# Kernel tuning notes

Hardware: AMD Instinct MI355X
Metric: run time of the kernel (lower is better)

Reference implementation:

```python
import jax, jax.numpy as jnp
import numpy as np
from jax import lax

POOL = 2048      # pool_size
HARD = 128       # hard_slices
EXTRA = 64       # random_extra
T_MIN, T_MAX, T_STEPS = -5.0, 5.0, 17
EPS = 1e-12


def _t_phi():
    t = jnp.linspace(T_MIN, T_MAX, T_STEPS)
    return t, jnp.exp(-0.5 * t * t)


def _slice_losses(z, A, t, phi):
    # z: [B, D], A: [D, M] -> per-slice ECF matching loss [M]
    zc = z - z.mean(axis=0, keepdims=True)
    u = zc @ A                              # [B, M]
    ut = u[:, :, None] * t                  # [B, M, T]
    ecf_re = jnp.cos(ut).mean(axis=0)       # [M, T] (= Re E[exp(i u t)])
    ecf_im = jnp.sin(ut).mean(axis=0)       # [M, T]
    integrand = ((ecf_re - phi) ** 2 + ecf_im ** 2) * phi
    dt = t[1:] - t[:-1]
    # trapezoid rule along t
    return (0.5 * (integrand[..., 1:] + integrand[..., :-1]) * dt).sum(axis=-1)


def _gram_schmidt(H):
    # Sequential Gram-Schmidt over columns of H: [D, m]. Mirrors
    # _gs_select_from_ranked in the generic case (unit random directions
    # never degenerate, so the top-m ranked columns are all kept).
    def body(j, Q):
        v = H[:, j]
        v = v - Q @ (Q.T @ v)   # unfilled cols of Q are zero -> no-op
        n = jnp.linalg.norm(v)
        return Q.at[:, j].set(v / jnp.maximum(n, EPS))
    return lax.fori_loop(0, H.shape[1], body, jnp.zeros_like(H))


def setup_inputs() -> dict:
    key = jax.random.key(0)
    z = jax.random.normal(key, (2048, 1024), dtype=jnp.float32)
    return {"z": z, "seed": 0}


def reference(z, seed):
    B, D = z.shape
    t, phi = _t_phi()

    # random unit-norm direction pool (seeded)
    A_pool = jax.random.normal(jax.random.key(seed), (D, POOL), dtype=z.dtype)
    A_pool = A_pool / (jnp.linalg.norm(A_pool, axis=0, keepdims=True) + EPS)

    # rank slices by ECF loss, take hardest, orthonormalize (hardmaxqr)
    losses = _slice_losses(z, A_pool, t, phi)
    ranked = jnp.argsort(-losses)
    hard_raw = A_pool[:, ranked[:HARD]]     # [D, HARD]
    hard = _gram_schmidt(hard_raw)

    # random extra directions, orthogonalized against hard
    R = jax.random.normal(jax.random.key(seed + 9991), (D, EXTRA), dtype=z.dtype)
    R = R / (jnp.linalg.norm(R, axis=0, keepdims=True) + EPS)
    R = R - hard @ (hard.T @ R)
    R = R / (jnp.linalg.norm(R, axis=0, keepdims=True) + EPS)

    A_final = jnp.concatenate([hard, R], axis=1)   # [D, HARD+EXTRA]
    final_losses = _slice_losses(z, A_final, t, phi)
    return final_losses.mean() * B
```

## Files before the change

kernel.cpp:

```cpp
#include <hip/hip_runtime.h>
#include <cstdint>
#include <cstddef>


#define THREEFRY_PARTITIONABLE 1

static constexpr int B_ = 2048;
static constexpr int D_ = 1024;
static constexpr int P_ = 2048;
static constexpr int HARD_ = 128;
static constexpr int EXTRA_ = 64;
static constexpr int NF_ = 192;
static constexpr int TS_ = 17;

typedef short short8v __attribute__((ext_vector_type(8)));
typedef float f32x4v __attribute__((ext_vector_type(4)));


__device__ __forceinline__ void threefry2x32(uint32_t k0, uint32_t k1,
                                             uint32_t c0, uint32_t c1,
                                             uint32_t& o0, uint32_t& o1) {
  uint32_t ks0 = k0, ks1 = k1, ks2 = 0x1BD11BDAu ^ k0 ^ k1;
  uint32_t x0 = c0 + ks0;
  uint32_t x1 = c1 + ks1;
#define TF_ROT(r) { x0 += x1; x1 = (x1 << (r)) | (x1 >> (32 - (r))); x1 ^= x0; }
  TF_ROT(13) TF_ROT(15) TF_ROT(26) TF_ROT(6)
  x0 += ks1; x1 += ks2 + 1u;
  TF_ROT(17) TF_ROT(29) TF_ROT(16) TF_ROT(24)
  x0 += ks2; x1 += ks0 + 2u;
  TF_ROT(13) TF_ROT(15) TF_ROT(26) TF_ROT(6)
  x0 += ks0; x1 += ks1 + 3u;
  TF_ROT(17) TF_ROT(29) TF_ROT(16) TF_ROT(24)
  x0 += ks1; x1 += ks2 + 4u;
  TF_ROT(13) TF_ROT(15) TF_ROT(26) TF_ROT(6)
  x0 += ks2; x1 += ks0 + 5u;
#undef TF_ROT
  o0 = x0; o1 = x1;
}

__device__ __forceinline__ float bits_to_normal(uint32_t bits) {
  uint32_t fb = (bits >> 9) | 0x3f800000u;
  float f = __uint_as_float(fb) - 1.0f;
  const float lo = -0.99999994f;
  float u = f * 2.0f + lo;
  u = fmaxf(lo, u);
  float w = -log1pf(-u * u);
  float p;
  if (w < 5.0f) {
    w = w - 2.5f;
    p = 2.81022636e-08f;
    p = fmaf(p, w, 3.43273939e-07f);
    p = fmaf(p, w, -3.5233877e-06f);
    p = fmaf(p, w, -4.39150654e-06f);
    p = fmaf(p, w, 0.00021858087f);
    p = fmaf(p, w, -0.00125372503f);
    p = fmaf(p, w, -0.00417768164f);
    p = fmaf(p, w, 0.246640727f);
    p = fmaf(p, w, 1.50140941f);
  } else {
    w = sqrtf(w) - 3.0f;
    p = -0.000200214257f;
    p = fmaf(p, w, 0.000100950558f);
    p = fmaf(p, w, 0.00134934322f);
    p = fmaf(p, w, -0.00367342844f);
    p = fmaf(p, w, 0.00573950773f);
    p = fmaf(p, w, -0.0076224613f);
    p = fmaf(p, w, 0.00943887047f);
    p = fmaf(p, w, 1.00167406f);
    p = fmaf(p, w, 2.83297682f);
  }
  return ((float)1.4142135623730951) * (p * u);
}

__device__ __forceinline__ float tf_normal(uint32_t k0, uint32_t k1,
                                           uint32_t idx) {
#if THREEFRY_PARTITIONABLE
  uint32_t a, b;
  threefry2x32(k0, k1, 0u, idx, a, b);
  return bits_to_normal(a ^ b);
#endif
}


__global__ __launch_bounds__(256) void colsum_part_kernel(const float* __restrict__ Z,
                                                          float* __restrict__ part) {
  int col = blockIdx.x * 256 + threadIdx.x;
  int r0 = blockIdx.y * 64;
  float s = 0.f;
  for (int r = r0; r < r0 + 64; ++r) s += Z[(size_t)r * D_ + col];
  part[blockIdx.y * D_ + col] = s;
}

__global__ __launch_bounds__(256) void colmean_fin_kernel(const float* __restrict__ part,
                                                          float* __restrict__ mean) {
  int col = blockIdx.x * 256 + threadIdx.x;
  float s = 0.f;
  for (int rb = 0; rb < 32; ++rb) s += part[rb * D_ + col];
  mean[col] = s * (1.0f / (float)B_);
}

__global__ __launch_bounds__(256) void gen_pool_norm_kernel(float* __restrict__ AT,
                                                            const int* __restrict__ seedp) {
  const int p = blockIdx.x;
  const int tid = threadIdx.x;
  uint64_t s = (uint64_t)(int64_t)seedp[0];
  uint32_t k0 = (uint32_t)(s >> 32), k1 = (uint32_t)s;
  float v[4]; float ss = 0.f;
#pragma unroll
  for (int q = 0; q < 4; ++q) {
    int d = tid + 256 * q;
    uint32_t i = (uint32_t)((d << 11) + p);
    v[q] = tf_normal(k0, k1, i);
    ss = fmaf(v[q], v[q], ss);
  }
  __shared__ float red[256];
  red[tid] = ss;
  __syncthreads();
  for (int st = 128; st > 0; st >>= 1) { if (tid < st) red[tid] += red[tid + st]; __syncthreads(); }
  float denom = sqrtf(red[0]) + 1e-12f;
#pragma unroll
  for (int q = 0; q < 4; ++q) {
    int d = tid + 256 * q;
    AT[(size_t)p * D_ + d] = v[q] / denom;
  }
}

__global__ __launch_bounds__(256) void gen_R_norm_kernel(float* __restrict__ DIRS,
                                                         const int* __restrict__ seedp) {
  const int j = blockIdx.x;
  const int tid = threadIdx.x;
  uint64_t s = (uint64_t)((int64_t)seedp[0] + 9991);
  uint32_t k0 = (uint32_t)(s >> 32), k1 = (uint32_t)s;
  float v[4]; float ss = 0.f;
#pragma unroll
  for (int q = 0; q < 4; ++q) {
    int d = tid + 256 * q;
    uint32_t i = (uint32_t)((d << 6) + j);
    v[q] = tf_normal(k0, k1, i);
    ss = fmaf(v[q], v[q], ss);
  }
  __shared__ float red[256];
  red[tid] = ss;
  __syncthreads();
  for (int st = 128; st > 0; st >>= 1) { if (tid < st) red[tid] += red[tid + st]; __syncthreads(); }
  float denom = sqrtf(red[0]) + 1e-12f;
#pragma unroll
  for (int q = 0; q < 4; ++q) {
    int d = tid + 256 * q;
    DIRS[(size_t)(HARD_ + j) * D_ + d] = v[q] / denom;
  }
}

__global__ __launch_bounds__(256) void rownorm_kernel(float* __restrict__ Arows, int ncols) {
  float* r = Arows + (size_t)blockIdx.x * ncols;
  int tid = threadIdx.x;
  float ss = 0.f;
  for (int d = tid; d < ncols; d += 256) { float v = r[d]; ss = fmaf(v, v, ss); }
  __shared__ float red[256];
  red[tid] = ss;
  __syncthreads();
  for (int s = 128; s > 0; s >>= 1) { if (tid < s) red[tid] += red[tid + s]; __syncthreads(); }
  float denom = sqrtf(red[0]) + 1e-12f;
  for (int d = tid; d < ncols; d += 256) r[d] = r[d] / denom;
}

__device__ __forceinline__ uint32_t f2bf_rne(float x) {
  uint32_t u = __float_as_uint(x);
  return (u + 0x7fffu + ((u >> 16) & 1u)) >> 16;
}

__global__ __launch_bounds__(512) void gemm_mfma_kernel(const float* __restrict__ A,
                                                        const float* __restrict__ Z,
                                                        const float* __restrict__ meanp,
                                                        float* __restrict__ C) {
  constexpr int BK = 32;
  __shared__ ushort Ah[128][40], Al[128][40], Bh[128][40], Bl[128][40];
  const int tid = threadIdx.x;
  const int lane = tid & 63;
  const int w = tid >> 6;
  const int wr = w >> 2;
  const int wc = w & 3;
  const int m0 = blockIdx.y * 128;
  const int n0 = blockIdx.x * 128;

  f32x4v acc[4][2];
#pragma unroll
  for (int mi = 0; mi < 4; ++mi)
#pragma unroll
    for (int ni = 0; ni < 2; ++ni) acc[mi][ni] = (f32x4v){0.f, 0.f, 0.f, 0.f};

  float4 ra[2], rb[2];
  auto ld = [&](int s) {
    const int k0 = s * BK;
#pragma unroll
    for (int q = 0; q < 2; ++q) {
      int f4 = tid + q * 512;
      int r = f4 >> 3;
      int kq = (f4 & 7) * 4;
      ra[q] = *(const float4*)(A + (size_t)(m0 + r) * D_ + k0 + kq);
      float4 z = *(const float4*)(Z + (size_t)(n0 + r) * D_ + k0 + kq);
      float4 mu = *(const float4*)(meanp + k0 + kq);
      rb[q] = make_float4(z.x - mu.x, z.y - mu.y, z.z - mu.z, z.w - mu.w);
    }
  };
  auto st = [&]() {
#pragma unroll
    for (int q = 0; q < 2; ++q) {
      int f4 = tid + q * 512;
      int r = f4 >> 3;
      int kq = (f4 & 7) * 4;
      float av[4] = {ra[q].x, ra[q].y, ra[q].z, ra[q].w};
      float bv[4] = {rb[q].x, rb[q].y, rb[q].z, rb[q].w};
      ushort ah[4], al[4], bh[4], bl[4];
#pragma unroll
      for (int c = 0; c < 4; ++c) {
        uint32_t h = f2bf_rne(av[c]);
        ah[c] = (ushort)h;
        al[c] = (ushort)f2bf_rne(av[c] - __uint_as_float(h << 16));
        uint32_t g = f2bf_rne(bv[c]);
        bh[c] = (ushort)g;
        bl[c] = (ushort)f2bf_rne(bv[c] - __uint_as_float(g << 16));
      }
      *(ushort4*)&Ah[r][kq] = make_ushort4(ah[0], ah[1], ah[2], ah[3]);
      *(ushort4*)&Al[r][kq] = make_ushort4(al[0], al[1], al[2], al[3]);
      *(ushort4*)&Bh[r][kq] = make_ushort4(bh[0], bh[1], bh[2], bh[3]);
      *(ushort4*)&Bl[r][kq] = make_ushort4(bl[0], bl[1], bl[2], bl[3]);
    }
  };
  auto compute = [&]() {
    const int rl = lane & 15;
    const int koff = (lane >> 4) * 8;
    short8v a_h[4], a_l[4], b_h[2], b_l[2];
#pragma unroll
    for (int mi = 0; mi < 4; ++mi) {
      int arow = wr * 64 + mi * 16 + rl;
      a_h[mi] = *(const short8v*)&Ah[arow][koff];
      a_l[mi] = *(const short8v*)&Al[arow][koff];
    }
#pragma unroll
    for (int ni = 0; ni < 2; ++ni) {
      int brow = wc * 32 + ni * 16 + rl;
      b_h[ni] = *(const short8v*)&Bh[brow][koff];
      b_l[ni] = *(const short8v*)&Bl[brow][koff];
    }
#pragma unroll
    for (int mi = 0; mi < 4; ++mi)
#pragma unroll
      for (int ni = 0; ni < 2; ++ni) {
        acc[mi][ni] = __builtin_amdgcn_mfma_f32_16x16x32_bf16(a_h[mi], b_h[ni], acc[mi][ni], 0, 0, 0);
        acc[mi][ni] = __builtin_amdgcn_mfma_f32_16x16x32_bf16(a_h[mi], b_l[ni], acc[mi][ni], 0, 0, 0);
        acc[mi][ni] = __builtin_amdgcn_mfma_f32_16x16x32_bf16(a_l[mi], b_h[ni], acc[mi][ni], 0, 0, 0);
      }
  };

  const int nst = D_ / BK;
  ld(0);
  for (int s = 0; s < nst; ++s) {
    if (s) __syncthreads();
    st();
    __syncthreads();
    if (s + 1 < nst) ld(s + 1);
    compute();
  }

  const int rl = lane & 15;
  const int rq = (lane >> 4) * 4;
#pragma unroll
  for (int mi = 0; mi < 4; ++mi)
#pragma unroll
    for (int ni = 0; ni < 2; ++ni) {
      int col = n0 + wc * 32 + ni * 16 + rl;
#pragma unroll
      for (int r = 0; r < 4; ++r) {
        int row = m0 + wr * 64 + mi * 16 + rq + r;
        C[(size_t)row * B_ + col] = acc[mi][ni][r];
      }
    }
}

template <int BM, int BN, int BK, int TM, int TN, int NT, bool CENTER_B>
__global__ __launch_bounds__(NT) void gemm_nt_kernel(const float* __restrict__ A,
                                                     const float* __restrict__ Bm,
                                                     const float* __restrict__ meanp,
                                                     float* __restrict__ C,
                                                     int M, int N, int K,
                                                     int lda, int ldb, int ldc) {
  static_assert(TN == 4 || TN == 8, "");
  static_assert((BM * BK) % (4 * NT) == 0, "");
  __shared__ float As[2][BK][BM + 4];
  __shared__ float Bs[2][BK][BN + 4];
  const int tid = threadIdx.x;
  constexpr int TX = BN / TN;
  constexpr int TY = NT / TX;
  static_assert(TY * TM == BM, "");
  const int tx = tid % TX;
  const int ty = tid / TX;
  const int m0 = blockIdx.y * BM;
  const int n0 = blockIdx.x * BN;
  constexpr int NF4 = (BM * BK) / (4 * NT);
  constexpr int F4R = BK / 4;

  float acc[TM][TN];
#pragma unroll
  for (int i = 0; i < TM; ++i)
#pragma unroll
    for (int j = 0; j < TN; ++j) acc[i][j] = 0.f;

  float4 ra[NF4], rb[NF4];

  auto ldnext = [&](int k0) {
#pragma unroll
    for (int q = 0; q < NF4; ++q) {
      int idx = tid + q * NT;
      int r = idx / F4R;
      int kk = (idx % F4R) * 4;
      ra[q] = *(const float4*)(A + (size_t)(m0 + r) * lda + k0 + kk);
      float4 b = *(const float4*)(Bm + (size_t)(n0 + r) * ldb + k0 + kk);
      if constexpr (CENTER_B) {
        float4 mu = *(const float4*)(meanp + k0 + kk);
        b = make_float4(b.x - mu.x, b.y - mu.y, b.z - mu.z, b.w - mu.w);
      }
      rb[q] = b;
    }
  };
  auto stnext = [&](int buf) {
#pragma unroll
    for (int q = 0; q < NF4; ++q) {
      int idx = tid + q * NT;
      int r = idx / F4R;
      int kk = (idx % F4R) * 4;
      As[buf][kk + 0][r] = ra[q].x; As[buf][kk + 1][r] = ra[q].y;
      As[buf][kk + 2][r] = ra[q].z; As[buf][kk + 3][r] = ra[q].w;
      Bs[buf][kk + 0][r] = rb[q].x; Bs[buf][kk + 1][r] = rb[q].y;
      Bs[buf][kk + 2][r] = rb[q].z; Bs[buf][kk + 3][r] = rb[q].w;
    }
  };
  auto compute = [&](int buf) {
#pragma unroll
    for (int kk = 0; kk < BK; ++kk) {
      float a[TM], b[TN];
#pragma unroll
      for (int q = 0; q < TM / 4; ++q) {
        float4 v = *(const float4*)&As[buf][kk][ty * TM + q * 4];
        a[q * 4 + 0] = v.x; a[q * 4 + 1] = v.y; a[q * 4 + 2] = v.z; a[q * 4 + 3] = v.w;
      }
      {
        float4 v = *(const float4*)&Bs[buf][kk][tx * 4];
        b[0] = v.x; b[1] = v.y; b[2] = v.z; b[3] = v.w;
      }
      if constexpr (TN == 8) {
        float4 v = *(const float4*)&Bs[buf][kk][BN / 2 + tx * 4];
        b[4] = v.x; b[5] = v.y; b[6] = v.z; b[7] = v.w;
      }
#pragma unroll
      for (int i = 0; i < TM; ++i)
#pragma unroll
        for (int j = 0; j < TN; ++j) acc[i][j] = fmaf(a[i], b[j], acc[i][j]);
    }
  };

  ldnext(0);
  stnext(0);
  __syncthreads();
  const int nst = K / BK;
  for (int s = 0; s < nst; ++s) {
    const int cur = s & 1;
    if (s + 1 < nst) ldnext((s + 1) * BK);
    compute(cur);
    if (s + 1 < nst) stnext(cur ^ 1);
    __syncthreads();
  }

#pragma unroll
  for (int i = 0; i < TM; ++i) {
    const int gm = m0 + ty * TM + i;
    float4 c0 = make_float4(acc[i][0], acc[i][1], acc[i][2], acc[i][3]);
    *(float4*)(C + (size_t)gm * ldc + n0 + tx * 4) = c0;
    if constexpr (TN == 8) {
      float4 c1 = make_float4(acc[i][4], acc[i][5], acc[i][6], acc[i][7]);
      *(float4*)(C + (size_t)gm * ldc + n0 + BN / 2 + tx * 4) = c1;
    }
  }
}

__global__ __launch_bounds__(256) void gram_kernel(const float* __restrict__ A,
                                                   const float* __restrict__ Bm,
                                                   float* __restrict__ C,
                                                   int K, int ldc) {
  __shared__ float As[32][136];
  __shared__ float BsT[128][36];
  const int tid = threadIdx.x;
  const int i0 = blockIdx.y * 32;
  const int j0 = blockIdx.x * 32;
  const int i = tid >> 3;
  const int jl = (tid & 7) * 4;

  float s[4][4];
#pragma unroll
  for (int m = 0; m < 4; ++m)
#pragma unroll
    for (int c = 0; c < 4; ++c) s[m][c] = 0.f;

  for (int kc = 0; kc < K; kc += 128) {
#pragma unroll
    for (int q = 0; q < 4; ++q) {
      int f4 = tid + 256 * q;
      int r = f4 >> 5;
      int kq = (f4 & 31) * 4;
      float4 va = *(const float4*)(A + (size_t)(i0 + r) * K + kc + kq);
      *(float4*)&As[r][kq] = va;
      float4 vb = *(const float4*)(Bm + (size_t)(j0 + r) * K + kc + kq);
      BsT[kq + 0][r] = vb.x; BsT[kq + 1][r] = vb.y;
      BsT[kq + 2][r] = vb.z; BsT[kq + 3][r] = vb.w;
    }
    __syncthreads();
    for (int k4 = 0; k4 < 128; k4 += 4) {
#pragma unroll
      for (int c = 0; c < 4; ++c) {
        int k = k4 + c;
        float a = As[i][k];
        float4 b = *(const float4*)&BsT[k][jl];
        s[0][c] = fmaf(a, b.x, s[0][c]);
        s[1][c] = fmaf(a, b.y, s[1][c]);
        s[2][c] = fmaf(a, b.z, s[2][c]);
        s[3][c] = fmaf(a, b.w, s[3][c]);
      }
    }
    __syncthreads();
  }
#pragma unroll
  for (int m = 0; m < 4; ++m)
    C[(size_t)(i0 + i) * ldc + j0 + jl + m] = (s[m][0] + s[m][1]) + (s[m][2] + s[m][3]);
}

__global__ __launch_bounds__(256) void ecf_loss_kernel(const float* __restrict__ U,
                                                       float* __restrict__ out_loss) {
  const float* u = U + (size_t)blockIdx.x * B_;
  const int tid = threadIdx.x;
  float sc[TS_], ss[TS_];
#pragma unroll
  for (int k = 0; k < TS_; ++k) { sc[k] = 0.f; ss[k] = 0.f; }

  for (int b = tid; b < B_; b += 256) {
    float x = u[b];
#pragma unroll
    for (int k = 0; k < TS_; ++k) {
      const double tk = -5.0 + 0.625 * (double)k;
      const float trev = (float)(tk * 0.15915494309189535);
      float r = x * trev;
      sc[k] += __builtin_amdgcn_cosf(r);
      ss[k] += __builtin_amdgcn_sinf(r);
    }
  }
#pragma unroll
  for (int k = 0; k < TS_; ++k) {
#pragma unroll
    for (int off = 32; off > 0; off >>= 1) {
      sc[k] += __shfl_down(sc[k], off, 64);
      ss[k] += __shfl_down(ss[k], off, 64);
    }
  }
  __shared__ float rsc[4][TS_], rss[4][TS_];
  int wid = tid >> 6, lane = tid & 63;
  if (lane == 0) {
#pragma unroll
    for (int k = 0; k < TS_; ++k) { rsc[wid][k] = sc[k]; rss[wid][k] = ss[k]; }
  }
  __syncthreads();
  if (tid == 0) {
    float loss = 0.f, prevI = 0.f;
#pragma unroll
    for (int k = 0; k < TS_; ++k) {
      float tk = -5.0f + 0.625f * (float)k;
      float phik = expf(-0.5f * tk * tk);
      float S = (rsc[0][k] + rsc[1][k]) + (rsc[2][k] + rsc[3][k]);
      float T = (rss[0][k] + rss[1][k]) + (rss[2][k] + rss[3][k]);
      float re = S * (1.0f / (float)B_) - phik;
      float im = T * (1.0f / (float)B_);
      float I = (re * re + im * im) * phik;
      if (k > 0) loss += 0.5f * (I + prevI) * 0.625f;
      prevI = I;
    }
    out_loss[blockIdx.x] = loss;
  }
}

__global__ __launch_bounds__(1024) void sort_kernel(const float* __restrict__ loss,
                                                    int* __restrict__ ranked) {
  __shared__ float ls[P_];
  __shared__ int li[P_];
  int tid = threadIdx.x;
  for (int i = tid; i < P_; i += 1024) { ls[i] = loss[i]; li[i] = i; }
  __syncthreads();
  for (int k = 2; k <= P_; k <<= 1) {
    for (int j = k >> 1; j > 0; j >>= 1) {
      for (int i = tid; i < P_; i += 1024) {
        int ixj = i ^ j;
        if (ixj > i) {
          bool up = ((i & k) == 0);
          float la = ls[i], lb = ls[ixj];
          int ia = li[i], ib = li[ixj];
          bool a_after_b = (la < lb) || (la == lb && ia > ib);
          bool sw = up ? a_after_b : (!a_after_b && !(la == lb && ia == ib));
          if (sw) { ls[i] = lb; ls[ixj] = la; li[i] = ib; li[ixj] = ia; }
        }
      }
      __syncthreads();
    }
  }
  for (int i = tid; i < P_; i += 1024) ranked[i] = li[i];
}

__global__ __launch_bounds__(256) void gather_ht_kernel(const float* __restrict__ AT,
                                                        const int* __restrict__ ranked,
                                                        float* __restrict__ HT) {
  int j = blockIdx.x;
  int src = ranked[j];
  for (int d = threadIdx.x; d < D_; d += 256)
    HT[(size_t)j * D_ + d] = AT[(size_t)src * D_ + d];
}

__global__ __launch_bounds__(512) void chol_inv_kernel(const float* __restrict__ G,
                                                       float* __restrict__ W) {
  __shared__ float g[HARD_][HARD_ + 1];
  __shared__ float w[HARD_][HARD_ + 1];
  __shared__ float m[16][16 * 7 + 4];
  __shared__ float rinv[HARD_];
  const int tid = threadIdx.x;

  for (int idx = tid; idx < HARD_ * HARD_; idx += 512)
    g[idx >> 7][idx & 127] = G[idx];
  for (int idx = tid; idx < HARD_ * (HARD_ + 1); idx += 512)
    (&w[0][0])[idx] = 0.f;
  __syncthreads();

  const int bcol = tid & 127;
  const int aoff = tid >> 7;
  for (int K = 0; K < 8; ++K) {
    const int b = K << 4;
    const int c0 = b + 16;
    const int nc = HARD_ - c0;

    if (tid < 16) {
      const int j = tid;
      float c[16];
#pragma unroll
      for (int k = 0; k < 16; ++k) c[k] = g[b + k][b + j];
#pragma unroll
      for (int i = 0; i < 16; ++i) {
        float rii = sqrtf(__shfl(c[i], i, 16));
        float rinvi = 1.0f / rii;
        float rij = c[i] * rinvi;
        if (j > i) c[i] = rij;
        if (j == i) c[i] = rii;
#pragma unroll
        for (int a = i + 1; a < 16; ++a) {
          float ria = __shfl(c[i], a, 16);
          if (j >= a) c[a] = fmaf(-ria, rij, c[a]);
        }
      }
#pragma unroll
      for (int k = 0; k < 16; ++k) if (k <= j) g[b + k][b + j] = c[k];
      rinv[b + j] = 1.0f / c[j];
    }
    __syncthreads();

    if (nc > 0) {
      if (tid < nc) {
        const int j = c0 + tid;
        float x[16];
#pragma unroll
        for (int i = 0; i < 16; ++i) {
          float acc = g[b + i][j];
#pragma unroll
          for (int m2 = 0; m2 < i; ++m2)
            acc = fmaf(-g[b + m2][b + i], x[m2], acc);
          x[i] = acc * rinv[b + i];
        }
#pragma unroll
        for (int i = 0; i < 16; ++i) g[b + i][j] = x[i];
      }
      __syncthreads();

      if (bcol >= c0) {
        float rkb[16];
#pragma unroll
        for (int k = 0; k < 16; ++k) rkb[k] = g[b + k][bcol];
        for (int a = c0 + aoff; a <= bcol; a += 4) {
          float acc = g[a][bcol];
#pragma unroll
          for (int k = 0; k < 16; ++k)
            acc = fmaf(-g[b + k][a], rkb[k], acc);
          g[a][bcol] = acc;
        }
      }
    }
    __syncthreads();
  }

  if (tid < HARD_) {
    const int blk = tid >> 4, j = tid & 15, b = blk << 4;
    const float myrinv = rinv[b + j];
    float wcol[16];
#pragma unroll
    for (int i = 15; i >= 0; --i) {
      float s = 0.f;
#pragma unroll
      for (int k = 15; k > i; --k) s = fmaf(g[b + i][b + k], wcol[k], s);
      float v = -rinv[b + i] * s;
      wcol[i] = (i < j) ? v : ((i == j) ? myrinv : 0.f);
    }
#pragma unroll
    for (int k = 0; k < 16; ++k) w[b + k][b + j] = wcol[k];
  }
  __syncthreads();

  for (int I = 6; I >= 0; --I) {
    const int b = I << 4;
    const int c0 = b + 16;
    const int nc = HARD_ - c0;
    const int nel = 16 * nc;
    for (int e = tid; e < nel; e += 512) {
      int r = e / nc, c = e - r * nc;
      float acc = 0.f;
      for (int k = c0; k < HARD_; ++k)
        acc = fmaf(g[b + r][k], w[k][c0 + c], acc);
      m[r][c] = acc;
    }
    __syncthreads();
    for (int e = tid; e < nel; e += 512) {
      int r = e / nc, c = e - r * nc;
      float acc = 0.f;
#pragma unroll
      for (int rp = 0; rp < 16; ++rp)
        acc = fmaf(w[b + r][b + rp], m[rp][c], acc);
      w[b + r][c0 + c] = -acc;
    }
    __syncthreads();
  }

  for (int idx = tid; idx < HARD_ * HARD_; idx += 512)
    W[idx] = w[idx >> 7][idx & 127];
}

__global__ __launch_bounds__(128) void apply_winv_kernel(const float* __restrict__ HT,
                                                         const float* __restrict__ W,
                                                         float* __restrict__ DIRS) {
  int j = blockIdx.y;
  int d = blockIdx.x * 128 + threadIdx.x;
  __shared__ float wc[HARD_];
  for (int i = threadIdx.x; i <= j; i += 128) wc[i] = W[i * HARD_ + j];
  __syncthreads();
  float acc = 0.f;
  for (int i = 0; i <= j; ++i) acc = fmaf(wc[i], HT[(size_t)i * D_ + d], acc);
  DIRS[(size_t)j * D_ + d] = acc;
}

__global__ __launch_bounds__(128) void proj_update_kernel(float* __restrict__ DIRS,
                                                          const float* __restrict__ C) {
  int j = blockIdx.y;
  int d = blockIdx.x * 128 + threadIdx.x;
  __shared__ float cc[HARD_];
  cc[threadIdx.x] = C[threadIdx.x * EXTRA_ + j];
  if (threadIdx.x + 128 < HARD_) cc[threadIdx.x + 128] = C[(threadIdx.x + 128) * EXTRA_ + j];
  __syncthreads();
  float acc = DIRS[(size_t)(HARD_ + j) * D_ + d];
  for (int i = 0; i < HARD_; ++i) acc = fmaf(-cc[i], DIRS[(size_t)i * D_ + d], acc);
  DIRS[(size_t)(HARD_ + j) * D_ + d] = acc;
}

__global__ __launch_bounds__(256) void finalize_kernel(const float* __restrict__ FL,
                                                       float* __restrict__ out) {
  __shared__ float red[256];
  int tid = threadIdx.x;
  red[tid] = (tid < NF_) ? FL[tid] : 0.f;
  __syncthreads();
  for (int s = 128; s > 0; s >>= 1) { if (tid < s) red[tid] += red[tid + s]; __syncthreads(); }
  if (tid == 0) out[0] = (red[0] / (float)NF_) * (float)B_;
}


extern "C" void kernel_launch(void* const* d_in, const int* in_sizes, int n_in,
                              void* d_out, int out_size, void* d_ws, size_t ws_size,
                              hipStream_t stream) {
  const float* Z = (const float*)d_in[0];
  const int* seedp = (const int*)d_in[1];
  float* out = (float*)d_out;
  (void)in_sizes; (void)n_in; (void)out_size; (void)ws_size;

  char* ws = (char*)d_ws;
  size_t off = 0;
  auto alloc = [&](size_t bytes) -> char* {
    char* p = ws + off;
    off += (bytes + 255) & ~(size_t)255;
    return p;
  };
  float* AT   = (float*)alloc((size_t)P_ * D_ * 4);
  float* UT   = (float*)alloc((size_t)P_ * B_ * 4);
  float* LOSS = (float*)alloc(P_ * 4);
  int*   IDX  = (int*)  alloc(P_ * 4);
  float* HT   = (float*)alloc((size_t)HARD_ * D_ * 4);
  float* G    = (float*)alloc(HARD_ * HARD_ * 4);
  float* W    = (float*)alloc(HARD_ * HARD_ * 4);
  float* DIRS = (float*)alloc((size_t)NF_ * D_ * 4);
  float* PRJ  = (float*)alloc(HARD_ * EXTRA_ * 4);
  float* UF   = (float*)alloc((size_t)NF_ * B_ * 4);
  float* FL   = (float*)alloc(NF_ * 4);
  float* PART = (float*)alloc(32 * D_ * 4);
  float* MEAN = (float*)alloc(D_ * 4);

  colsum_part_kernel<<<dim3(D_ / 256, 32), 256, 0, stream>>>(Z, PART);
  colmean_fin_kernel<<<D_ / 256, 256, 0, stream>>>(PART, MEAN);

  gen_pool_norm_kernel<<<P_, 256, 0, stream>>>(AT, seedp);

  gemm_mfma_kernel<<<dim3(B_ / 128, P_ / 128), 512, 0, stream>>>(AT, Z, MEAN, UT);
  ecf_loss_kernel<<<P_, 256, 0, stream>>>(UT, LOSS);

  sort_kernel<<<1, 1024, 0, stream>>>(LOSS, IDX);
  gather_ht_kernel<<<HARD_, 256, 0, stream>>>(AT, IDX, HT);

  gram_kernel<<<dim3(HARD_ / 32, HARD_ / 32), 256, 0, stream>>>(HT, HT, G, D_, HARD_);
  chol_inv_kernel<<<1, 512, 0, stream>>>(G, W);
  apply_winv_kernel<<<dim3(D_ / 128, HARD_), 128, 0, stream>>>(HT, W, DIRS);

  gen_R_norm_kernel<<<EXTRA_, 256, 0, stream>>>(DIRS, seedp);
  gram_kernel<<<dim3(EXTRA_ / 32, HARD_ / 32), 256, 0, stream>>>(
      DIRS, DIRS + (size_t)HARD_ * D_, PRJ, D_, EXTRA_);
  proj_update_kernel<<<dim3(D_ / 128, EXTRA_), 128, 0, stream>>>(DIRS, PRJ);
  rownorm_kernel<<<EXTRA_, 256, 0, stream>>>(DIRS + (size_t)HARD_ * D_, D_);

  gemm_nt_kernel<64, 64, 32, 4, 4, 256, true><<<dim3(B_ / 64, NF_ / 64), 256, 0, stream>>>(
      DIRS, Z, MEAN, UF, NF_, B_, D_, D_, D_, B_);
  ecf_loss_kernel<<<NF_, 256, 0, stream>>>(UF, FL);
  finalize_kernel<<<1, 256, 0, stream>>>(FL, out);
}
```

Measured before the change: 431.2 us.

## Derive final projections from pool projections via triangular transform instead of recomputing GEMM

Instead of building the orthonormal directions explicitly and running a second GEMM against Z, the final projections are computed algebraically. The hard slices come from applying the inverse Cholesky factor W to the already-computed pool projections UT. The extra slices are projected by a small GEMM done alongside the pool GEMM, then corrected using W^T*(H^T R) coefficients, with the norm derived from 1 - ||P||^2. This removes the apply_winv, proj_update, rownorm and the final 192-direction GEMM over the full D, but relies on the orthonormality identity for normalization, which can shift numerics.

```diff
diff --git a/kernel.cpp b/kernel.cpp
--- a/kernel.cpp
+++ b/kernel.cpp
@@ -74,11 +74,9 @@
 
 __device__ __forceinline__ float tf_normal(uint32_t k0, uint32_t k1,
                                            uint32_t idx) {
-#if THREEFRY_PARTITIONABLE
   uint32_t a, b;
   threefry2x32(k0, k1, 0u, idx, a, b);
   return bits_to_normal(a ^ b);
-#endif
 }
 
 
@@ -125,7 +123,7 @@
   }
 }
 
-__global__ __launch_bounds__(256) void gen_R_norm_kernel(float* __restrict__ DIRS,
+__global__ __launch_bounds__(256) void gen_R_norm_kernel(float* __restrict__ AT,
                                                          const int* __restrict__ seedp) {
   const int j = blockIdx.x;
   const int tid = threadIdx.x;
@@ -147,21 +145,8 @@
 #pragma unroll
   for (int q = 0; q < 4; ++q) {
     int d = tid + 256 * q;
-    DIRS[(size_t)(HARD_ + j) * D_ + d] = v[q] / denom;
-  }
-}
-
-__global__ __launch_bounds__(256) void rownorm_kernel(float* __restrict__ Arows, int ncols) {
-  float* r = Arows + (size_t)blockIdx.x * ncols;
-  int tid = threadIdx.x;
-  float ss = 0.f;
-  for (int d = tid; d < ncols; d += 256) { float v = r[d]; ss = fmaf(v, v, ss); }
-  __shared__ float red[256];
-  red[tid] = ss;
-  __syncthreads();
-  for (int s = 128; s > 0; s >>= 1) { if (tid < s) red[tid] += red[tid + s]; __syncthreads(); }
-  float denom = sqrtf(red[0]) + 1e-12f;
-  for (int d = tid; d < ncols; d += 256) r[d] = r[d] / denom;
+    AT[(size_t)(P_ + j) * D_ + d] = v[q] / denom;
+  }
 }
 
 __device__ __forceinline__ uint32_t f2bf_rne(float x) {
@@ -623,6 +608,7 @@
     for (int e = tid; e < nel; e += 512) {
       int r = e / nc, c = e - r * nc;
       float acc = 0.f;
+#pragma unroll 8
       for (int k = c0; k < HARD_; ++k)
         acc = fmaf(g[b + r][k], w[k][c0 + c], acc);
       m[r][c] = acc;
@@ -643,30 +629,93 @@
     W[idx] = w[idx >> 7][idx & 127];
 }
 
-__global__ __launch_bounds__(128) void apply_winv_kernel(const float* __restrict__ HT,
-                                                         const float* __restrict__ W,
-                                                         float* __restrict__ DIRS) {
-  int j = blockIdx.y;
-  int d = blockIdx.x * 128 + threadIdx.x;
-  __shared__ float wc[HARD_];
-  for (int i = threadIdx.x; i <= j; i += 128) wc[i] = W[i * HARD_ + j];
-  __syncthreads();
-  float acc = 0.f;
-  for (int i = 0; i <= j; ++i) acc = fmaf(wc[i], HT[(size_t)i * D_ + d], acc);
-  DIRS[(size_t)j * D_ + d] = acc;
-}
-
-__global__ __launch_bounds__(128) void proj_update_kernel(float* __restrict__ DIRS,
-                                                          const float* __restrict__ C) {
-  int j = blockIdx.y;
-  int d = blockIdx.x * 128 + threadIdx.x;
-  __shared__ float cc[HARD_];
-  cc[threadIdx.x] = C[threadIdx.x * EXTRA_ + j];
-  if (threadIdx.x + 128 < HARD_) cc[threadIdx.x + 128] = C[(threadIdx.x + 128) * EXTRA_ + j];
-  __syncthreads();
-  float acc = DIRS[(size_t)(HARD_ + j) * D_ + d];
-  for (int i = 0; i < HARD_; ++i) acc = fmaf(-cc[i], DIRS[(size_t)i * D_ + d], acc);
-  DIRS[(size_t)(HARD_ + j) * D_ + d] = acc;
+__global__ __launch_bounds__(512) void wtrans_kernel(const float* __restrict__ W,
+                                                     const float* __restrict__ GHR,
+                                                     float* __restrict__ PRJp,
+                                                     float* __restrict__ RNORM) {
+  __shared__ float wsh[HARD_][HARD_];
+  __shared__ float gsh[HARD_][EXTRA_];
+  __shared__ float psh[HARD_][EXTRA_];
+  const int tid = threadIdx.x;
+  for (int e = tid; e < HARD_ * HARD_; e += 512) wsh[e >> 7][e & 127] = W[e];
+  for (int e = tid; e < HARD_ * EXTRA_; e += 512) gsh[e >> 6][e & 63] = GHR[e];
+  __syncthreads();
+  const int j = tid & 63;
+  const int ig = tid >> 6;
+#pragma unroll
+  for (int q = 0; q < 16; ++q) {
+    const int i = ig * 16 + q;
+    float acc = 0.f;
+    for (int k = 0; k <= i; ++k)
+      acc = fmaf(wsh[k][i], gsh[k][j], acc);
+    psh[i][j] = acc;
+    PRJp[i * EXTRA_ + j] = acc;
+  }
+  __syncthreads();
+  if (tid < EXTRA_) {
+    float s = 0.f;
+    for (int i = 0; i < HARD_; ++i) { float p = psh[i][tid]; s = fmaf(p, p, s); }
+    float n = sqrtf(fmaxf(1.f - s, 0.f));
+    RNORM[tid] = 1.f / (n + 1e-12f);
+  }
+}
+
+__global__ __launch_bounds__(256) void uq_kernel(const float* __restrict__ W,
+                                                 const float* __restrict__ UT,
+                                                 const int* __restrict__ ranked,
+                                                 float* __restrict__ UF) {
+  __shared__ float wt[HARD_][16];
+  __shared__ int rk[HARD_];
+  const int tid = threadIdx.x;
+  const int j0 = blockIdx.y * 16;
+  const int n0 = blockIdx.x * 256;
+  for (int e = tid; e < HARD_ * 16; e += 256) {
+    int i = e >> 4, jj = e & 15;
+    wt[i][jj] = W[i * HARD_ + j0 + jj];
+  }
+  if (tid < HARD_) rk[tid] = ranked[tid];
+  __syncthreads();
+  float acc[16];
+#pragma unroll
+  for (int jj = 0; jj < 16; ++jj) acc[jj] = 0.f;
+  const int imax = j0 + 16;
+  for (int i = 0; i < imax; ++i) {
+    float u = UT[(size_t)rk[i] * B_ + n0 + tid];
+#pragma unroll
+    for (int jj = 0; jj < 16; ++jj) acc[jj] = fmaf(wt[i][jj], u, acc[jj]);
+  }
+#pragma unroll
+  for (int jj = 0; jj < 16; ++jj)
+    UF[(size_t)(j0 + jj) * B_ + n0 + tid] = acc[jj];
+}
+
+__global__ __launch_bounds__(256) void uproj_kernel(const float* __restrict__ PRJp,
+                                                    const float* __restrict__ RNORM,
+                                                    const float* __restrict__ UREXT,
+                                                    float* __restrict__ UF) {
+  __shared__ float pc[HARD_][16];
+  __shared__ float rn[16];
+  const int tid = threadIdx.x;
+  const int j0 = blockIdx.y * 16;
+  const int n0 = blockIdx.x * 256;
+  for (int e = tid; e < HARD_ * 16; e += 256) {
+    int i = e >> 4, jj = e & 15;
+    pc[i][jj] = PRJp[i * EXTRA_ + j0 + jj];
+  }
+  if (tid < 16) rn[tid] = RNORM[j0 + tid];
+  __syncthreads();
+  float acc[16];
+#pragma unroll
+  for (int jj = 0; jj < 16; ++jj)
+    acc[jj] = UREXT[(size_t)(j0 + jj) * B_ + n0 + tid];
+  for (int i = 0; i < HARD_; ++i) {
+    float u = UF[(size_t)i * B_ + n0 + tid];
+#pragma unroll
+    for (int jj = 0; jj < 16; ++jj) acc[jj] = fmaf(-pc[i][jj], u, acc[jj]);
+  }
+#pragma unroll
+  for (int jj = 0; jj < 16; ++jj)
+    UF[(size_t)(HARD_ + j0 + jj) * B_ + n0 + tid] = acc[jj] * rn[jj];
 }
 
 __global__ __launch_bounds__(256) void finalize_kernel(const float* __restrict__ FL,
@@ -695,43 +744,45 @@
     off += (bytes + 255) & ~(size_t)255;
     return p;
   };
-  float* AT   = (float*)alloc((size_t)P_ * D_ * 4);
-  float* UT   = (float*)alloc((size_t)P_ * B_ * 4);
-  float* LOSS = (float*)alloc(P_ * 4);
-  int*   IDX  = (int*)  alloc(P_ * 4);
-  float* HT   = (float*)alloc((size_t)HARD_ * D_ * 4);
-  float* G    = (float*)alloc(HARD_ * HARD_ * 4);
-  float* W    = (float*)alloc(HARD_ * HARD_ * 4);
-  float* DIRS = (float*)alloc((size_t)NF_ * D_ * 4);
-  float* PRJ  = (float*)alloc(HARD_ * EXTRA_ * 4);
-  float* UF   = (float*)alloc((size_t)NF_ * B_ * 4);
-  float* FL   = (float*)alloc(NF_ * 4);
-  float* PART = (float*)alloc(32 * D_ * 4);
-  float* MEAN = (float*)alloc(D_ * 4);
+  float* AT    = (float*)alloc((size_t)(P_ + EXTRA_) * D_ * 4);
+  float* UT    = (float*)alloc((size_t)P_ * B_ * 4);
+  float* LOSS  = (float*)alloc(P_ * 4);
+  int*   IDX   = (int*)  alloc(P_ * 4);
+  float* HT    = (float*)alloc((size_t)HARD_ * D_ * 4);
+  float* G     = (float*)alloc(HARD_ * HARD_ * 4);
+  float* W     = (float*)alloc(HARD_ * HARD_ * 4);
+  float* GHR   = (float*)alloc(HARD_ * EXTRA_ * 4);
+  float* PRJp  = (float*)alloc(HARD_ * EXTRA_ * 4);
+  float* RNORM = (float*)alloc(EXTRA_ * 4);
+  float* UREXT = (float*)alloc((size_t)EXTRA_ * B_ * 4);
+  float* UF    = (float*)alloc((size_t)NF_ * B_ * 4);
+  float* FL    = (float*)alloc(NF_ * 4);
+  float* PART  = (float*)alloc(32 * D_ * 4);
+  float* MEAN  = (float*)alloc(D_ * 4);
 
   colsum_part_kernel<<<dim3(D_ / 256, 32), 256, 0, stream>>>(Z, PART);
   colmean_fin_kernel<<<D_ / 256, 256, 0, stream>>>(PART, MEAN);
 
   gen_pool_norm_kernel<<<P_, 256, 0, stream>>>(AT, seedp);
+  gen_R_norm_kernel<<<EXTRA_, 256, 0, stream>>>(AT, seedp);
 
   gemm_mfma_kernel<<<dim3(B_ / 128, P_ / 128), 512, 0, stream>>>(AT, Z, MEAN, UT);
+  gemm_nt_kernel<64, 64, 32, 4, 4, 256, true><<<dim3(B_ / 64, 1), 256, 0, stream>>>(
+      AT + (size_t)P_ * D_, Z, MEAN, UREXT, EXTRA_, B_, D_, D_, D_, B_);
+
   ecf_loss_kernel<<<P_, 256, 0, stream>>>(UT, LOSS);
-
   sort_kernel<<<1, 1024, 0, stream>>>(LOSS, IDX);
   gather_ht_kernel<<<HARD_, 256, 0, stream>>>(AT, IDX, HT);
 
   gram_kernel<<<dim3(HARD_ / 32, HARD_ / 32), 256, 0, stream>>>(HT, HT, G, D_, HARD_);
   chol_inv_kernel<<<1, 512, 0, stream>>>(G, W);
-  apply_winv_kernel<<<dim3(D_ / 128, HARD_), 128, 0, stream>>>(HT, W, DIRS);
-
-  gen_R_norm_kernel<<<EXTRA_, 256, 0, stream>>>(DIRS, seedp);
   gram_kernel<<<dim3(EXTRA_ / 32, HARD_ / 32), 256, 0, stream>>>(
-      DIRS, DIRS + (size_t)HARD_ * D_, PRJ, D_, EXTRA_);
-  proj_update_kernel<<<dim3(D_ / 128, EXTRA_), 128, 0, stream>>>(DIRS, PRJ);
-  rownorm_kernel<<<EXTRA_, 256, 0, stream>>>(DIRS + (size_t)HARD_ * D_, D_);
-
-  gemm_nt_kernel<64, 64, 32, 4, 4, 256, true><<<dim3(B_ / 64, NF_ / 64), 256, 0, stream>>>(
-      DIRS, Z, MEAN, UF, NF_, B_, D_, D_, D_, B_);
+      HT, AT + (size_t)P_ * D_, GHR, D_, EXTRA_);
+  wtrans_kernel<<<1, 512, 0, stream>>>(W, GHR, PRJp, RNORM);
+
+  uq_kernel<<<dim3(B_ / 256, HARD_ / 16), 256, 0, stream>>>(W, UT, IDX, UF);
+  uproj_kernel<<<dim3(B_ / 256, EXTRA_ / 16), 256, 0, stream>>>(PRJp, RNORM, UREXT, UF);
+
   ecf_loss_kernel<<<NF_, 256, 0, stream>>>(UF, FL);
   finalize_kernel<<<1, 256, 0, stream>>>(FL, out);
 }
```

Measured after the change: 490.6 us. 1.14x slower.
